# Kernel tuning notes

Hardware: AMD Instinct MI355X
Metric: run time of the kernel (lower is better)

The kernel has to match this reference:

```python
import jax, jax.numpy as jnp
import numpy as np
import math

D_MODEL = 1024
N_HEAD = 16
D_HEAD = D_MODEL // N_HEAD


def setup_inputs() -> dict:
    key = jax.random.key(0)
    k0, k1, k2, k3, k4 = jax.random.split(key, 5)
    B, N = 4, 2048
    inp = jax.random.normal(k0, (B, N, D_MODEL), dtype=jnp.float32)
    # causal mask: True = keep (masked_fill on ~mask)
    mask = jnp.tril(jnp.ones((N, N), dtype=bool))
    # qkv_proj Linear(d_model, 3*d_model); output Linear(d_model, d_model)
    s_in = 1.0 / math.sqrt(D_MODEL)
    W_qkv = jax.random.uniform(k1, (D_MODEL, 3 * D_MODEL), jnp.float32, -s_in, s_in)
    b_qkv = jax.random.uniform(k2, (3 * D_MODEL,), jnp.float32, -s_in, s_in)
    W_out = jax.random.uniform(k3, (D_MODEL, D_MODEL), jnp.float32, -s_in, s_in)
    b_out = jax.random.uniform(k4, (D_MODEL,), jnp.float32, -s_in, s_in)
    return {"input": inp, "W_qkv": W_qkv, "b_qkv": b_qkv,
            "W_out": W_out, "b_out": b_out, "mask": mask}


def reference(input, W_qkv, b_qkv, W_out, b_out, mask):
    B, N, d = input.shape
    qkv = input @ W_qkv + b_qkv                       # [B,N,3d]  (dropout=eval no-op)
    q, k, v = jnp.split(qkv, 3, axis=-1)
    # [B,N,H,Dh] -> [B,H,N,Dh]
    q = q.reshape(B, N, N_HEAD, D_HEAD).transpose(0, 2, 1, 3)
    k = k.reshape(B, N, N_HEAD, D_HEAD).transpose(0, 2, 1, 3)
    v = v.reshape(B, N, N_HEAD, D_HEAD).transpose(0, 2, 1, 3)
    scale = 1.0 / math.sqrt(D_HEAD)
    scores = jnp.einsum('bhqd,bhkd->bhqk', q, k) * scale   # [B,H,N,N]
    scores = jnp.where(mask, scores, -jnp.inf)
    attn = jax.nn.softmax(scores, axis=-1)
    out = jnp.einsum('bhqk,bhkd->bhqd', attn, v)           # [B,H,N,Dh]
    out = out.transpose(0, 2, 1, 3).reshape(B, N, d)       # concat heads
    return out @ W_out + b_out
```

## Files before the change

### kernel.cpp

```cpp
#include <hip/hip_runtime.h>
#include <hip/hip_bf16.h>

typedef unsigned short u16;
typedef unsigned u32;
typedef __attribute__((ext_vector_type(4))) unsigned short u16x4;
typedef __attribute__((ext_vector_type(8))) unsigned short u16x8;
typedef __attribute__((ext_vector_type(4))) unsigned u32x4;
typedef __attribute__((ext_vector_type(8))) __bf16 bf16x8;
typedef __attribute__((ext_vector_type(4))) float f32x4;

typedef __attribute__((address_space(1))) void as1v;
typedef __attribute__((address_space(3))) void as3v;

#define MFMA16(a, b, c) __builtin_amdgcn_mfma_f32_16x16x32_bf16(a, b, c, 0, 0, 0)

#if __has_builtin(__builtin_amdgcn_permlane16_swap) && __has_builtin(__builtin_amdgcn_permlane32_swap)
#define HAVE_PERMLANE_SWAP 1
#else
#define HAVE_PERMLANE_SWAP 0
#endif

__device__ __forceinline__ u16 f2bf(float f) {
    unsigned u = __builtin_bit_cast(unsigned, f);
    u += 0x7fffu + ((u >> 16) & 1u);
    return (u16)(u >> 16);
}

__device__ __forceinline__ float bf2f(u16 v) {
    u32 u = ((u32)v) << 16;
    return __builtin_bit_cast(float, u);
}

__device__ __forceinline__ u32 pkbf(float lo, float hi) {
    u32 r;
    asm("v_cvt_pk_bf16_f32 %0, %1, %2" : "=v"(r) : "v"(lo), "v"(hi));
    return r;
}

__device__ __forceinline__ void gload16(const void* g, void* l) {
    __builtin_amdgcn_global_load_lds((as1v*)g, (as3v*)l, 16, 0, 0);
}

__device__ __forceinline__ float redmax_cross(float v) {
#if HAVE_PERMLANE_SWAP
    u32 xu = __builtin_bit_cast(u32, v);
    auto r16 = __builtin_amdgcn_permlane16_swap(xu, xu, false, false);
    float a = fmaxf(__builtin_bit_cast(float, (u32)r16[0]),
                    __builtin_bit_cast(float, (u32)r16[1]));
    u32 au = __builtin_bit_cast(u32, a);
    auto r32 = __builtin_amdgcn_permlane32_swap(au, au, false, false);
    return fmaxf(__builtin_bit_cast(float, (u32)r32[0]),
                 __builtin_bit_cast(float, (u32)r32[1]));
#else
    v = fmaxf(v, __shfl_xor(v, 16, 64));
    return fmaxf(v, __shfl_xor(v, 32, 64));
#endif
}

__device__ __forceinline__ float redsum_cross(float v) {
#if HAVE_PERMLANE_SWAP
    u32 xu = __builtin_bit_cast(u32, v);
    auto r16 = __builtin_amdgcn_permlane16_swap(xu, xu, false, false);
    float a = __builtin_bit_cast(float, (u32)r16[0]) +
              __builtin_bit_cast(float, (u32)r16[1]);
    u32 au = __builtin_bit_cast(u32, a);
    auto r32 = __builtin_amdgcn_permlane32_swap(au, au, false, false);
    return __builtin_bit_cast(float, (u32)r32[0]) +
           __builtin_bit_cast(float, (u32)r32[1]);
#else
    v += __shfl_xor(v, 16, 64);
    return v + __shfl_xor(v, 32, 64);
#endif
}

__global__ void convert_f32_bf16(const float* __restrict__ in, u16* __restrict__ out, int n4) {
    int i = blockIdx.x * blockDim.x + threadIdx.x;
    if (i < n4) {
        float4 v = *(const float4*)&in[(size_t)i * 4];
        u16x4 o;
        o.x = f2bf(v.x); o.y = f2bf(v.y); o.z = f2bf(v.z); o.w = f2bf(v.w);
        *(u16x4*)&out[(size_t)i * 4] = o;
    }
}

__global__ void transpose_convert(const float* __restrict__ in, u16* __restrict__ out, int R, int C) {
    __shared__ float tl[64][65];
    const int rb = blockIdx.x, cb = blockIdx.y;
    const int tid = threadIdx.x;
    for (int it = 0; it < 4; ++it) {
        int lin = (tid + it * 256) * 4;
        int r = lin >> 6, c = lin & 63;
        float4 v = *(const float4*)&in[(size_t)(rb * 64 + r) * C + cb * 64 + c];
        tl[r][c + 0] = v.x; tl[r][c + 1] = v.y; tl[r][c + 2] = v.z; tl[r][c + 3] = v.w;
    }
    __syncthreads();
    for (int it = 0; it < 4; ++it) {
        int lin = (tid + it * 256) * 4;
        int oc = lin >> 6, orr = lin & 63;
        u16x4 o;
        o.x = f2bf(tl[orr + 0][oc]);
        o.y = f2bf(tl[orr + 1][oc]);
        o.z = f2bf(tl[orr + 2][oc]);
        o.w = f2bf(tl[orr + 3][oc]);
        *(u16x4*)&out[(size_t)(cb * 64 + oc) * R + rb * 64 + orr] = o;
    }
}

__global__ __launch_bounds__(256, 3) void gemm128_qkv(
    const u16* __restrict__ A, const u16* __restrict__ Bt, const float* __restrict__ bias,
    u16* __restrict__ qb, u16* __restrict__ kb, u16* __restrict__ vtb) {
    constexpr int K = 1024;
    constexpr int NT = 32;
    __shared__ u16 ldsu[24576];

    const int bid = blockIdx.x;
    const int s = (bid & 7) * 192 + (bid >> 3);
    const int bm = s / 24, bn = s % 24;

    const int tid = threadIdx.x, wid = tid >> 6, lane = tid & 63;
    const int wr = wid >> 1, wc = wid & 1;
    const int l15 = lane & 15, lhi = lane >> 4;

    const int sslot = (lane & 7) ^ (lane >> 3);
    const int kcol = (sslot & 3) * 8;
    const int mloc = (lane >> 3) * 2 + (sslot >> 2);

    const u16* Arow[2];
    const u16* Brow[2];
#pragma unroll
    for (int li = 0; li < 2; ++li) {
        int sg = wid * 2 + li;
        Arow[li] = A + (size_t)(bm * 128 + sg * 16 + mloc) * K + kcol;
        Brow[li] = Bt + (size_t)(bn * 128 + sg * 16 + mloc) * K + kcol;
    }

    auto stageA = [&](int buf, int t) {
#pragma unroll
        for (int li = 0; li < 2; ++li) {
            int sg = wid * 2 + li;
            gload16(Arow[li] + t * 32, (char*)ldsu + buf * 16384 + sg * 1024);
        }
    };
    auto stageB = [&](int buf, int t) {
#pragma unroll
        for (int li = 0; li < 2; ++li) {
            int sg = wid * 2 + li;
            gload16(Brow[li] + t * 32, (char*)ldsu + buf * 16384 + 8192 + sg * 1024);
        }
    };

    const int rslot = ((l15 & 1) * 4 + lhi) ^ ((l15 >> 1) & 7);
    const int fragoff = (l15 >> 1) * 64 + rslot * 8;

    f32x4 acc[4][4];
#pragma unroll
    for (int i = 0; i < 4; ++i)
#pragma unroll
        for (int j = 0; j < 4; ++j) acc[i][j] = (f32x4){0.f, 0.f, 0.f, 0.f};

    auto doTile = [&](int cur, int tstage, bool dostage) {
        const u16* Ab = ldsu + cur * 8192 + wr * 2048 + fragoff;
        const u16* Bb = ldsu + cur * 8192 + 4096 + wc * 2048 + fragoff;
        bf16x8 af[4], b0, b1;
#pragma unroll
        for (int mf = 0; mf < 4; ++mf) af[mf] = *(const bf16x8*)(Ab + mf * 512);
        b0 = *(const bf16x8*)(Bb);
        b1 = *(const bf16x8*)(Bb + 512);
        if (dostage) stageA(tstage % 3, tstage);
        __builtin_amdgcn_s_setprio(1);
#pragma unroll
        for (int mf = 0; mf < 4; ++mf) {
            acc[mf][0] = MFMA16(af[mf], b0, acc[mf][0]);
            acc[mf][1] = MFMA16(af[mf], b1, acc[mf][1]);
        }
        __builtin_amdgcn_s_setprio(0);
        b0 = *(const bf16x8*)(Bb + 1024);
        b1 = *(const bf16x8*)(Bb + 1536);
        if (dostage) stageB(tstage % 3, tstage);
        __builtin_amdgcn_s_setprio(1);
#pragma unroll
        for (int mf = 0; mf < 4; ++mf) {
            acc[mf][2] = MFMA16(af[mf], b0, acc[mf][2]);
            acc[mf][3] = MFMA16(af[mf], b1, acc[mf][3]);
        }
        __builtin_amdgcn_s_setprio(0);
    };

    stageA(0, 0); stageB(0, 0);
    stageA(1, 1); stageB(1, 1);
    asm volatile("s_waitcnt vmcnt(4)" ::: "memory");
    __builtin_amdgcn_s_barrier();
    __builtin_amdgcn_sched_barrier(0);

    for (int t = 0; t < NT - 2; ++t) {
        doTile(t % 3, t + 2, true);
        asm volatile("s_waitcnt vmcnt(4)" ::: "memory");
        __builtin_amdgcn_s_barrier();
        __builtin_amdgcn_sched_barrier(0);
    }
    doTile((NT - 2) % 3, 0, false);
    asm volatile("s_waitcnt vmcnt(0)" ::: "memory");
    __builtin_amdgcn_s_barrier();
    __builtin_amdgcn_sched_barrier(0);
    doTile((NT - 1) % 3, 0, false);

    const int cg0 = bn * 128 + wc * 64;
    const int which = cg0 >> 10, rem = cg0 & 1023;
    const int hh = rem >> 6, dh0 = rem & 63;
    const int rgb0 = bm * 128 + wr * 64;
    const int bb = rgb0 >> 11, n0 = rgb0 & 2047;

    if (which == 2) {
        const size_t vbase = ((size_t)(bb * 16 + hh) * 64 + dh0) * 2048 + (size_t)n0;
#pragma unroll
        for (int nt = 0; nt < 4; ++nt) {
            float bv = bias[cg0 + nt * 16 + l15];
            size_t rowb = vbase + (size_t)(nt * 16 + l15) * 2048;
#pragma unroll
            for (int mt = 0; mt < 4; ++mt) {
                u16x4 w;
#pragma unroll
                for (int v = 0; v < 4; ++v) w[v] = f2bf(acc[mt][nt][v] + bv);
                *(u16x4*)&vtb[rowb + mt * 16 + lhi * 4] = w;
            }
        }
    } else {
        u16* dst = (which == 0) ? qb : kb;
        const float qs = (which == 0) ? 0.18033688011112042f : 1.0f;
        const size_t gbase = (((size_t)bb * 16 + hh) * 2048 + n0) * 64 + dh0;
#pragma unroll
        for (int nt = 0; nt < 4; ++nt) {
            float bv = bias[cg0 + nt * 16 + l15];
#pragma unroll
            for (int mt = 0; mt < 4; ++mt)
#pragma unroll
                for (int v = 0; v < 4; ++v) {
                    int n = mt * 16 + lhi * 4 + v;
                    dst[gbase + (size_t)n * 64 + nt * 16 + l15] =
                        f2bf((acc[mt][nt][v] + bv) * qs);
                }
        }
    }
}

__global__ __launch_bounds__(512, 2) void gemm256_out(
    const u16* __restrict__ A, const u16* __restrict__ Bt, const float* __restrict__ bias,
    float* __restrict__ outf) {
    constexpr int K = 1024;
    constexpr int NT = 32;
    __shared__ u16 ldsu[49152];

    const int bid = blockIdx.x;
    const int swz = (bid & 7) * 32 + (bid >> 3);
    const int bm = swz >> 3, bn = swz & 7;

    const int tid = threadIdx.x, wid = tid >> 6, lane = tid & 63;
    const int wr = wid >> 2, wc = wid & 3;
    const int l15 = lane & 15, lhi = lane >> 4;

    const int sslot = (lane & 7) ^ (lane >> 3);
    const int kcol = (sslot & 3) * 8;
    const int mloc = (lane >> 3) * 2 + (sslot >> 2);

    const u16* Arow[2];
#pragma unroll
    for (int li = 0; li < 2; ++li) {
        int sg = wid * 2 + li;
        Arow[li] = A + (size_t)(bm * 256 + sg * 16 + mloc) * K + kcol;
    }
    const u16* Brow = Bt + (size_t)(bn * 128 + wid * 16 + mloc) * K + kcol;

    auto stageA = [&](int buf, int t) {
#pragma unroll
        for (int li = 0; li < 2; ++li) {
            int sg = wid * 2 + li;
            gload16(Arow[li] + t * 32, (char*)ldsu + buf * 24576 + sg * 1024);
        }
    };
    auto stageB = [&](int buf, int t) {
        gload16(Brow + t * 32, (char*)ldsu + buf * 24576 + 16384 + wid * 1024);
    };

    const int rslot = ((l15 & 1) * 4 + lhi) ^ ((l15 >> 1) & 7);
    const int fragoff = (l15 >> 1) * 64 + rslot * 8;

    f32x4 acc[8][2];
#pragma unroll
    for (int i = 0; i < 8; ++i) {
        acc[i][0] = (f32x4){0.f, 0.f, 0.f, 0.f};
        acc[i][1] = (f32x4){0.f, 0.f, 0.f, 0.f};
    }

    auto doTile = [&](int cur, int tstage, bool dostage) {
        const u16* Ab = ldsu + cur * 12288 + wr * 4096 + fragoff;
        const u16* Bb = ldsu + cur * 12288 + 8192 + wc * 1024 + fragoff;
        bf16x8 af[8], b0, b1;
#pragma unroll
        for (int mf = 0; mf < 8; ++mf) af[mf] = *(const bf16x8*)(Ab + mf * 512);
        b0 = *(const bf16x8*)(Bb);
        b1 = *(const bf16x8*)(Bb + 512);
        if (dostage) stageA(tstage & 3, tstage);
        __builtin_amdgcn_s_setprio(1);
#pragma unroll
        for (int mf = 0; mf < 8; ++mf) acc[mf][0] = MFMA16(af[mf], b0, acc[mf][0]);
        __builtin_amdgcn_s_setprio(0);
        if (dostage) stageB(tstage & 3, tstage);
        __builtin_amdgcn_s_setprio(1);
#pragma unroll
        for (int mf = 0; mf < 8; ++mf) acc[mf][1] = MFMA16(af[mf], b1, acc[mf][1]);
        __builtin_amdgcn_s_setprio(0);
    };

    stageA(0, 0); stageB(0, 0);
    stageA(1, 1); stageB(1, 1);
    stageA(2, 2); stageB(2, 2);
    asm volatile("s_waitcnt vmcnt(6)" ::: "memory");
    __builtin_amdgcn_s_barrier();
    __builtin_amdgcn_sched_barrier(0);

    for (int t = 0; t < NT - 3; ++t) {
        doTile(t & 3, t + 3, true);
        asm volatile("s_waitcnt vmcnt(6)" ::: "memory");
        __builtin_amdgcn_s_barrier();
        __builtin_amdgcn_sched_barrier(0);
    }
    doTile((NT - 3) & 3, 0, false);
    asm volatile("s_waitcnt vmcnt(3)" ::: "memory");
    __builtin_amdgcn_s_barrier();
    __builtin_amdgcn_sched_barrier(0);
    doTile((NT - 2) & 3, 0, false);
    asm volatile("s_waitcnt vmcnt(0)" ::: "memory");
    __builtin_amdgcn_s_barrier();
    __builtin_amdgcn_sched_barrier(0);
    doTile((NT - 1) & 3, 0, false);

#pragma unroll
    for (int nf = 0; nf < 2; ++nf) {
        int cg = bn * 128 + wc * 32 + nf * 16 + l15;
        float bv = bias[cg];
#pragma unroll
        for (int mf = 0; mf < 8; ++mf) {
            int rgb = bm * 256 + wr * 128 + mf * 16 + lhi * 4;
#pragma unroll
            for (int v = 0; v < 4; ++v)
                outf[(size_t)(rgb + v) * 1024 + cg] = acc[mf][nf][v] + bv;
        }
    }
}

__global__ __launch_bounds__(256, 4) void attn_kernel(
    const u16* __restrict__ qbuf, const u16* __restrict__ kbuf,
    const u16* __restrict__ vtb, u16* __restrict__ obuf,
    float* __restrict__ pbufA, float* __restrict__ mlbuf) {
    __shared__ u16 Kl[2][64 * 64];
    __shared__ u16 Vl[2][64 * 64];
    const int bid = blockIdx.x;
    const int bh = ((bid & 7) << 3) + ((bid >> 3) & 7);
    const int piece = bid >> 6;
    const int half = piece & 1;
    const int p = piece >> 1;
    const int b = bh >> 4, h = bh & 15;
    const int tid = threadIdx.x, wid = tid >> 6, lane = tid & 63;
    const int l15 = lane & 15, lhi = lane >> 4;

    const int srow = lane >> 3;
    const int scolb = ((lane & 7) * 16) ^ (srow << 4);

    auto stage = [&](int buf, int t) {
        const int kbase = t * 64;
#pragma unroll
        for (int s = 0; s < 2; ++s) {
            int sg = wid * 2 + s;
            int row = sg * 8 + srow;
            const u16* gk = kbuf + ((size_t)bh * 2048 + kbase + row) * 64 + (scolb >> 1);
            gload16(gk, (char*)Kl[buf] + sg * 1024);
            const u16* gv = vtb + ((size_t)bh * 64 + row) * 2048 + kbase + (scolb >> 1);
            gload16(gv, (char*)Vl[buf] + sg * 1024);
        }
    };

    auto run_piece = [&](int c, int t0, int t1, int mode) {
        const int q0 = c * 128 + wid * 32;
        bf16x8 qf0[2], qf1[2];
        {
            const u16* qp0 = qbuf + ((size_t)bh * 2048 + q0 + l15) * 64 + lhi * 8;
            const u16* qp1 = qbuf + ((size_t)bh * 2048 + q0 + 16 + l15) * 64 + lhi * 8;
            qf0[0] = *(const bf16x8*)(qp0); qf0[1] = *(const bf16x8*)(qp0 + 32);
            qf1[0] = *(const bf16x8*)(qp1); qf1[1] = *(const bf16x8*)(qp1 + 32);
        }
        float m0 = -1e30f, l0 = 0.f, m1 = -1e30f, l1 = 0.f;
        f32x4 o0[4], o1[4];
#pragma unroll
        for (int d = 0; d < 4; ++d) {
            o0[d] = (f32x4){0.f, 0.f, 0.f, 0.f};
            o1[d] = (f32x4){0.f, 0.f, 0.f, 0.f};
        }
        const int ntW = 2 * c + (wid >> 1) + 1;

        auto smax = [&](f32x4* s, int qg0, int t, float& m, float& l, f32x4* oa, u32* pw) {
            const int qg = qg0 + l15;
            if (64 * t + 63 > qg0) {
#pragma unroll
                for (int kb4 = 0; kb4 < 4; ++kb4)
#pragma unroll
                    for (int v = 0; v < 4; ++v) {
                        int kg = 64 * t + kb4 * 16 + lhi * 4 + v;
                        if (kg > qg) s[kb4][v] = -1e30f;
                    }
            }
            float pm = fmaxf(fmaxf(fmaxf(s[0][0], s[0][1]), fmaxf(s[0][2], s[0][3])),
                             fmaxf(fmaxf(s[1][0], s[1][1]), fmaxf(s[1][2], s[1][3])));
            pm = fmaxf(pm, fmaxf(fmaxf(fmaxf(s[2][0], s[2][1]), fmaxf(s[2][2], s[2][3])),
                                 fmaxf(fmaxf(s[3][0], s[3][1]), fmaxf(s[3][2], s[3][3]))));
            pm = redmax_cross(pm);
            if (!__all(pm <= m + 8.f)) {
                float nm = fmaxf(m, pm);
                float f = exp2f(m - nm);
                m = nm;
                l *= f;
#pragma unroll
                for (int d = 0; d < 4; ++d)
#pragma unroll
                    for (int v = 0; v < 4; ++v) oa[d][v] *= f;
            }
            float rs = 0.f;
#pragma unroll
            for (int kb4 = 0; kb4 < 4; ++kb4)
#pragma unroll
                for (int v = 0; v < 4; ++v) {
                    float e = exp2f(s[kb4][v] - m);
                    s[kb4][v] = e;
                    rs += e;
                }
            l += redsum_cross(rs);
            pw[0] = pkbf(s[0][0], s[0][1]); pw[1] = pkbf(s[0][2], s[0][3]);
            pw[2] = pkbf(s[1][0], s[1][1]); pw[3] = pkbf(s[1][2], s[1][3]);
            pw[4] = pkbf(s[2][0], s[2][1]); pw[5] = pkbf(s[2][2], s[2][3]);
            pw[6] = pkbf(s[3][0], s[3][1]); pw[7] = pkbf(s[3][2], s[3][3]);
        };

        auto computeChunk = [&](const char* Kb, const char* Vb, int t) {
            f32x4 s0[4], s1[4];
            __builtin_amdgcn_s_setprio(1);
#pragma unroll
            for (int kb4 = 0; kb4 < 4; ++kb4) {
                const int r = kb4 * 16 + l15;
                const int sw = (r & 7) << 4;
                const int rowb = r * 128;
                bf16x8 kf0 = *(const bf16x8*)(Kb + rowb + ((lhi * 16) ^ sw));
                bf16x8 kf1 = *(const bf16x8*)(Kb + rowb + ((64 + lhi * 16) ^ sw));
                f32x4 a0 = (f32x4){0.f, 0.f, 0.f, 0.f};
                a0 = MFMA16(kf0, qf0[0], a0);
                a0 = MFMA16(kf1, qf0[1], a0);
                s0[kb4] = a0;
                f32x4 a1 = (f32x4){0.f, 0.f, 0.f, 0.f};
                a1 = MFMA16(kf0, qf1[0], a1);
                a1 = MFMA16(kf1, qf1[1], a1);
                s1[kb4] = a1;
            }
            __builtin_amdgcn_s_setprio(0);
            u32 pw0[8], pw1[8];
            smax(s0, q0, t, m0, l0, o0, pw0);
            smax(s1, q0 + 16, t, m1, l1, o1, pw1);
            __builtin_amdgcn_s_setprio(1);
#pragma unroll
            for (int ks = 0; ks < 2; ++ks) {
                bf16x8 pb0 = __builtin_bit_cast(bf16x8,
                    (u32x4){pw0[ks * 4 + 0], pw0[ks * 4 + 1], pw0[ks * 4 + 2], pw0[ks * 4 + 3]});
                bf16x8 pb1 = __builtin_bit_cast(bf16x8,
                    (u32x4){pw1[ks * 4 + 0], pw1[ks * 4 + 1], pw1[ks * 4 + 2], pw1[ks * 4 + 3]});
#pragma unroll
                for (int dhb = 0; dhb < 4; ++dhb) {
                    const int r = dhb * 16 + l15;
                    const int sw = (r & 7) << 4;
                    u16x4 v0 = *(const u16x4*)(Vb + r * 128 + ((ks * 64 + 8 * lhi) ^ sw));
                    u16x4 v1 = *(const u16x4*)(Vb + r * 128 + ((ks * 64 + 32 + 8 * lhi) ^ sw));
                    u16x8 vv = {v0[0], v0[1], v0[2], v0[3], v1[0], v1[1], v1[2], v1[3]};
                    bf16x8 vf = __builtin_bit_cast(bf16x8, vv);
                    o0[dhb] = MFMA16(vf, pb0, o0[dhb]);
                    o1[dhb] = MFMA16(vf, pb1, o1[dhb]);
                }
            }
            __builtin_amdgcn_s_setprio(0);
        };

        __syncthreads();
        stage(0, t0);
        int t = t0;
        for (;;) {
            __syncthreads();
            if (t + 1 < t1) stage(((t - t0) & 1) ^ 1, t + 1);
            if (t < ntW) computeChunk((const char*)Kl[(t - t0) & 1],
                                      (const char*)Vl[(t - t0) & 1], t);
            if (++t == t1) break;
        }

        const int pi = 15 - c;
        if (mode == 0) {
            auto epi = [&](int goff, float l, const f32x4* oa) {
                const float rl = 1.f / l;
                const int q = q0 + goff + l15;
                const size_t rowoff = ((size_t)b * 2048 + q) * 1024 + h * 64;
#pragma unroll
                for (int dhb = 0; dhb < 4; ++dhb) {
                    u16x4 w;
#pragma unroll
                    for (int v = 0; v < 4; ++v) w[v] = f2bf(oa[dhb][v] * rl);
                    *(u16x4*)&obuf[rowoff + dhb * 16 + lhi * 4] = w;
                }
            };
            epi(0, l0, o0);
            epi(16, l1, o1);
        } else if (mode == 1) {
            auto epi = [&](int goff, float m, float l, const f32x4* oa) {
                const int ql = wid * 32 + goff + l15;
                const size_t rowi = ((size_t)bh * 8 + pi) * 128 + ql;
                float* prow = pbufA + rowi * 64;
#pragma unroll
                for (int dhb = 0; dhb < 4; ++dhb)
                    *(f32x4*)&prow[dhb * 16 + lhi * 4] = oa[dhb];
                if (lhi == 0) { mlbuf[rowi] = m; mlbuf[65536 + rowi] = l; }
            };
            epi(0, m0, l0, o0);
            epi(16, m1, l1, o1);
        } else {
            auto epi = [&](int goff, float m, float l, const f32x4* oa) {
                const float rl = 1.f / l;
                const int q = q0 + goff + l15;
                const size_t rowoff = ((size_t)b * 2048 + q) * 1024 + h * 64;
#pragma unroll
                for (int dhb = 0; dhb < 4; ++dhb) {
                    u16x4 w;
#pragma unroll
                    for (int v = 0; v < 4; ++v) w[v] = f2bf(oa[dhb][v] * rl);
                    *(u16x4*)&obuf[rowoff + dhb * 16 + lhi * 4] = w;
                }
                const int ql = wid * 32 + goff + l15;
                const size_t rowi = ((size_t)bh * 8 + pi) * 128 + ql;
                if (lhi == 0) { mlbuf[131072 + rowi] = m; mlbuf[196608 + rowi] = l; }
            };
            epi(0, m0, l0, o0);
            epi(16, m1, l1, o1);
        }
    };

    if (half == 0) {
        run_piece(p, 0, 2 * p + 2, 0);
        run_piece(15 - p, 0, 15 - 2 * p, 1);
    } else {
        run_piece(15 - p, 15 - 2 * p, 32 - 2 * p, 2);
    }
}

__global__ __launch_bounds__(256) void merge_lse(
    const float* __restrict__ pbufA, const float* __restrict__ mlbuf,
    u16* __restrict__ obuf) {
    const int gid = blockIdx.x * 256 + threadIdx.x;
    const int rid = gid >> 2, seg = gid & 3;
    const float m1 = mlbuf[rid], l1 = mlbuf[65536 + rid];
    const float m2 = mlbuf[131072 + rid], l2 = mlbuf[196608 + rid];
    const float M = fmaxf(m1, m2);
    const float f1 = exp2f(m1 - M), f2 = exp2f(m2 - M);
    const float rden = 1.f / (l1 * f1 + l2 * f2);
    const float w2 = l2 * f2;
    const int bh = rid >> 10, rem = rid & 1023, pp = rem >> 7, ql = rem & 127;
    const int b = bh >> 4, h = bh & 15;
    const int qg = (15 - pp) * 128 + ql;
    u16* orow = obuf + ((size_t)b * 2048 + qg) * 1024 + h * 64 + seg * 16;
    const float* prow = pbufA + (size_t)rid * 64 + seg * 16;
#pragma unroll
    for (int j = 0; j < 4; ++j) {
        f32x4 o1 = *(const f32x4*)&prow[j * 4];
        u16x4 o2 = *(const u16x4*)&orow[j * 4];
        u16x4 w;
#pragma unroll
        for (int v = 0; v < 4; ++v)
            w[v] = f2bf((o1[v] * f1 + bf2f(o2[v]) * w2) * rden);
        *(u16x4*)&orow[j * 4] = w;
    }
}

extern "C" void kernel_launch(void* const* d_in, const int* in_sizes, int n_in,
                              void* d_out, int out_size, void* d_ws, size_t ws_size,
                              hipStream_t stream) {
    const float* inp   = (const float*)d_in[0];
    const float* W_qkv = (const float*)d_in[1];
    const float* b_qkv = (const float*)d_in[2];
    const float* W_out = (const float*)d_in[3];
    const float* b_out = (const float*)d_in[4];
    float* out = (float*)d_out;

    u16* xb   = (u16*)d_ws;
    u16* wqt  = xb + 8388608;
    u16* wot  = wqt + 3145728;
    u16* qbuf = wot + 1048576;
    u16* kbuf = qbuf + 8388608;
    u16* vtb  = kbuf + 8388608;
    u16* obuf = vtb + 8388608;
    float* pbufA = (float*)xb;
    float* mlbuf = (float*)wqt;

    convert_f32_bf16<<<8192, 256, 0, stream>>>(inp, xb, 2097152);
    transpose_convert<<<dim3(16, 48), 256, 0, stream>>>(W_qkv, wqt, 1024, 3072);
    transpose_convert<<<dim3(16, 16), 256, 0, stream>>>(W_out, wot, 1024, 1024);
    gemm128_qkv<<<1536, 256, 0, stream>>>(xb, wqt, b_qkv, qbuf, kbuf, vtb);
    attn_kernel<<<1024, 256, 0, stream>>>(qbuf, kbuf, vtb, obuf, pbufA, mlbuf);
    merge_lse<<<1024, 256, 0, stream>>>(pbufA, mlbuf, obuf);
    gemm256_out<<<256, 512, 0, stream>>>(obuf, wot, b_out, out);
}
```

Measured before the change: 201.6 us.

## Retile output GEMM to 128x128 blocks and store attention partials in bf16

The output projection GEMM moves from 256x128 tiles with 512 threads and 4 LDS buffers to 128x128 tiles with 256 threads, 3 LDS buffers and twice as many blocks. The aim is better occupancy and load balance across CUs. The split-attention partial outputs are now written as bf16 instead of fp32, which halves that traffic between the attention and merge kernels. Non-temporal loads and stores are used on these scratch buffers, at some precision cost for the partial accumulator.

After: 201.2 us. About the same (-0.2%).

```diff
diff --git a/kernel.cpp b/kernel.cpp
--- a/kernel.cpp
+++ b/kernel.cpp
@@ -243,19 +243,19 @@
     }
 }
 
-__global__ __launch_bounds__(512, 2) void gemm256_out(
+__global__ __launch_bounds__(256, 3) void gemm128_out(
     const u16* __restrict__ A, const u16* __restrict__ Bt, const float* __restrict__ bias,
     float* __restrict__ outf) {
     constexpr int K = 1024;
     constexpr int NT = 32;
-    __shared__ u16 ldsu[49152];
+    __shared__ u16 ldsu[24576];
 
     const int bid = blockIdx.x;
-    const int swz = (bid & 7) * 32 + (bid >> 3);
-    const int bm = swz >> 3, bn = swz & 7;
+    const int s = (bid & 7) * 64 + (bid >> 3);
+    const int bm = s >> 3, bn = s & 7;
 
     const int tid = threadIdx.x, wid = tid >> 6, lane = tid & 63;
-    const int wr = wid >> 2, wc = wid & 3;
+    const int wr = wid >> 1, wc = wid & 1;
     const int l15 = lane & 15, lhi = lane >> 4;
 
     const int sslot = (lane & 7) ^ (lane >> 3);
@@ -263,87 +263,94 @@
     const int mloc = (lane >> 3) * 2 + (sslot >> 2);
 
     const u16* Arow[2];
+    const u16* Brow[2];
 #pragma unroll
     for (int li = 0; li < 2; ++li) {
         int sg = wid * 2 + li;
-        Arow[li] = A + (size_t)(bm * 256 + sg * 16 + mloc) * K + kcol;
-    }
-    const u16* Brow = Bt + (size_t)(bn * 128 + wid * 16 + mloc) * K + kcol;
+        Arow[li] = A + (size_t)(bm * 128 + sg * 16 + mloc) * K + kcol;
+        Brow[li] = Bt + (size_t)(bn * 128 + sg * 16 + mloc) * K + kcol;
+    }
 
     auto stageA = [&](int buf, int t) {
 #pragma unroll
         for (int li = 0; li < 2; ++li) {
             int sg = wid * 2 + li;
-            gload16(Arow[li] + t * 32, (char*)ldsu + buf * 24576 + sg * 1024);
+            gload16(Arow[li] + t * 32, (char*)ldsu + buf * 16384 + sg * 1024);
         }
     };
     auto stageB = [&](int buf, int t) {
-        gload16(Brow + t * 32, (char*)ldsu + buf * 24576 + 16384 + wid * 1024);
+#pragma unroll
+        for (int li = 0; li < 2; ++li) {
+            int sg = wid * 2 + li;
+            gload16(Brow[li] + t * 32, (char*)ldsu + buf * 16384 + 8192 + sg * 1024);
+        }
     };
 
     const int rslot = ((l15 & 1) * 4 + lhi) ^ ((l15 >> 1) & 7);
     const int fragoff = (l15 >> 1) * 64 + rslot * 8;
 
-    f32x4 acc[8][2];
-#pragma unroll
-    for (int i = 0; i < 8; ++i) {
-        acc[i][0] = (f32x4){0.f, 0.f, 0.f, 0.f};
-        acc[i][1] = (f32x4){0.f, 0.f, 0.f, 0.f};
-    }
+    f32x4 acc[4][4];
+#pragma unroll
+    for (int i = 0; i < 4; ++i)
+#pragma unroll
+        for (int j = 0; j < 4; ++j) acc[i][j] = (f32x4){0.f, 0.f, 0.f, 0.f};
 
     auto doTile = [&](int cur, int tstage, bool dostage) {
-        const u16* Ab = ldsu + cur * 12288 + wr * 4096 + fragoff;
-        const u16* Bb = ldsu + cur * 12288 + 8192 + wc * 1024 + fragoff;
-        bf16x8 af[8], b0, b1;
-#pragma unroll
-        for (int mf = 0; mf < 8; ++mf) af[mf] = *(const bf16x8*)(Ab + mf * 512);
+        const u16* Ab = ldsu + cur * 8192 + wr * 2048 + fragoff;
+        const u16* Bb = ldsu + cur * 8192 + 4096 + wc * 2048 + fragoff;
+        bf16x8 af[4], b0, b1;
+#pragma unroll
+        for (int mf = 0; mf < 4; ++mf) af[mf] = *(const bf16x8*)(Ab + mf * 512);
         b0 = *(const bf16x8*)(Bb);
         b1 = *(const bf16x8*)(Bb + 512);
-        if (dostage) stageA(tstage & 3, tstage);
+        if (dostage) stageA(tstage % 3, tstage);
         __builtin_amdgcn_s_setprio(1);
 #pragma unroll
-        for (int mf = 0; mf < 8; ++mf) acc[mf][0] = MFMA16(af[mf], b0, acc[mf][0]);
+        for (int mf = 0; mf < 4; ++mf) {
+            acc[mf][0] = MFMA16(af[mf], b0, acc[mf][0]);
+            acc[mf][1] = MFMA16(af[mf], b1, acc[mf][1]);
+        }
         __builtin_amdgcn_s_setprio(0);
-        if (dostage) stageB(tstage & 3, tstage);
+        b0 = *(const bf16x8*)(Bb + 1024);
+        b1 = *(const bf16x8*)(Bb + 1536);
+        if (dostage) stageB(tstage % 3, tstage);
         __builtin_amdgcn_s_setprio(1);
 #pragma unroll
-        for (int mf = 0; mf < 8; ++mf) acc[mf][1] = MFMA16(af[mf], b1, acc[mf][1]);
+        for (int mf = 0; mf < 4; ++mf) {
+            acc[mf][2] = MFMA16(af[mf], b0, acc[mf][2]);
+            acc[mf][3] = MFMA16(af[mf], b1, acc[mf][3]);
+        }
         __builtin_amdgcn_s_setprio(0);
     };
 
     stageA(0, 0); stageB(0, 0);
     stageA(1, 1); stageB(1, 1);
-    stageA(2, 2); stageB(2, 2);
-    asm volatile("s_waitcnt vmcnt(6)" ::: "memory");
+    asm volatile("s_waitcnt vmcnt(4)" ::: "memory");
     __builtin_amdgcn_s_barrier();
     __builtin_amdgcn_sched_barrier(0);
 
-    for (int t = 0; t < NT - 3; ++t) {
-        doTile(t & 3, t + 3, true);
-        asm volatile("s_waitcnt vmcnt(6)" ::: "memory");
+    for (int t = 0; t < NT - 2; ++t) {
+        doTile(t % 3, t + 2, true);
+        asm volatile("s_waitcnt vmcnt(4)" ::: "memory");
         __builtin_amdgcn_s_barrier();
         __builtin_amdgcn_sched_barrier(0);
     }
-    doTile((NT - 3) & 3, 0, false);
-    asm volatile("s_waitcnt vmcnt(3)" ::: "memory");
-    __builtin_amdgcn_s_barrier();
-    __builtin_amdgcn_sched_barrier(0);
-    doTile((NT - 2) & 3, 0, false);
+    doTile((NT - 2) % 3, 0, false);
     asm volatile("s_waitcnt vmcnt(0)" ::: "memory");
     __builtin_amdgcn_s_barrier();
     __builtin_amdgcn_sched_barrier(0);
-    doTile((NT - 1) & 3, 0, false);
-
-#pragma unroll
-    for (int nf = 0; nf < 2; ++nf) {
-        int cg = bn * 128 + wc * 32 + nf * 16 + l15;
+    doTile((NT - 1) % 3, 0, false);
+
+#pragma unroll
+    for (int nt = 0; nt < 4; ++nt) {
+        int cg = bn * 128 + wc * 64 + nt * 16 + l15;
         float bv = bias[cg];
 #pragma unroll
-        for (int mf = 0; mf < 8; ++mf) {
-            int rgb = bm * 256 + wr * 128 + mf * 16 + lhi * 4;
+        for (int mt = 0; mt < 4; ++mt) {
+            int rg = bm * 128 + wr * 64 + mt * 16 + lhi * 4;
 #pragma unroll
             for (int v = 0; v < 4; ++v)
-                outf[(size_t)(rgb + v) * 1024 + cg] = acc[mf][nf][v] + bv;
+                outf[(size_t)(rg + v) * 1024 + cg] = acc[mt][nt][v] + bv;
         }
     }
 }
@@ -351,7 +358,7 @@
 __global__ __launch_bounds__(256, 4) void attn_kernel(
     const u16* __restrict__ qbuf, const u16* __restrict__ kbuf,
     const u16* __restrict__ vtb, u16* __restrict__ obuf,
-    float* __restrict__ pbufA, float* __restrict__ mlbuf) {
+    u16* __restrict__ pbufA, float* __restrict__ mlbuf) {
     __shared__ u16 Kl[2][64 * 64];
     __shared__ u16 Vl[2][64 * 64];
     const int bid = blockIdx.x;
@@ -515,11 +522,18 @@
             auto epi = [&](int goff, float m, float l, const f32x4* oa) {
                 const int ql = wid * 32 + goff + l15;
                 const size_t rowi = ((size_t)bh * 8 + pi) * 128 + ql;
-                float* prow = pbufA + rowi * 64;
-#pragma unroll
-                for (int dhb = 0; dhb < 4; ++dhb)
-                    *(f32x4*)&prow[dhb * 16 + lhi * 4] = oa[dhb];
-                if (lhi == 0) { mlbuf[rowi] = m; mlbuf[65536 + rowi] = l; }
+                u16* prow = pbufA + rowi * 64;
+#pragma unroll
+                for (int dhb = 0; dhb < 4; ++dhb) {
+                    u16x4 w;
+#pragma unroll
+                    for (int v = 0; v < 4; ++v) w[v] = f2bf(oa[dhb][v]);
+                    __builtin_nontemporal_store(w, (u16x4*)&prow[dhb * 16 + lhi * 4]);
+                }
+                if (lhi == 0) {
+                    __builtin_nontemporal_store(m, &mlbuf[rowi]);
+                    __builtin_nontemporal_store(l, &mlbuf[65536 + rowi]);
+                }
             };
             epi(0, m0, l0, o0);
             epi(16, m1, l1, o1);
@@ -537,7 +551,10 @@
                 }
                 const int ql = wid * 32 + goff + l15;
                 const size_t rowi = ((size_t)bh * 8 + pi) * 128 + ql;
-                if (lhi == 0) { mlbuf[131072 + rowi] = m; mlbuf[196608 + rowi] = l; }
+                if (lhi == 0) {
+                    __builtin_nontemporal_store(m, &mlbuf[131072 + rowi]);
+                    __builtin_nontemporal_store(l, &mlbuf[196608 + rowi]);
+                }
             };
             epi(0, m0, l0, o0);
             epi(16, m1, l1, o1);
@@ -553,12 +570,14 @@
 }
 
 __global__ __launch_bounds__(256) void merge_lse(
-    const float* __restrict__ pbufA, const float* __restrict__ mlbuf,
+    const u16* __restrict__ pbufA, const float* __restrict__ mlbuf,
     u16* __restrict__ obuf) {
     const int gid = blockIdx.x * 256 + threadIdx.x;
     const int rid = gid >> 2, seg = gid & 3;
-    const float m1 = mlbuf[rid], l1 = mlbuf[65536 + rid];
-    const float m2 = mlbuf[131072 + rid], l2 = mlbuf[196608 + rid];
+    const float m1 = __builtin_nontemporal_load(&mlbuf[rid]);
+    const float l1 = __builtin_nontemporal_load(&mlbuf[65536 + rid]);
+    const float m2 = __builtin_nontemporal_load(&mlbuf[131072 + rid]);
+    const float l2 = __builtin_nontemporal_load(&mlbuf[196608 + rid]);
     const float M = fmaxf(m1, m2);
     const float f1 = exp2f(m1 - M), f2 = exp2f(m2 - M);
     const float rden = 1.f / (l1 * f1 + l2 * f2);
@@ -567,15 +586,15 @@
     const int b = bh >> 4, h = bh & 15;
     const int qg = (15 - pp) * 128 + ql;
     u16* orow = obuf + ((size_t)b * 2048 + qg) * 1024 + h * 64 + seg * 16;
-    const float* prow = pbufA + (size_t)rid * 64 + seg * 16;
+    const u16* prow = pbufA + (size_t)rid * 64 + seg * 16;
 #pragma unroll
     for (int j = 0; j < 4; ++j) {
-        f32x4 o1 = *(const f32x4*)&prow[j * 4];
+        u16x4 p1 = __builtin_nontemporal_load((const u16x4*)&prow[j * 4]);
         u16x4 o2 = *(const u16x4*)&orow[j * 4];
         u16x4 w;
 #pragma unroll
         for (int v = 0; v < 4; ++v)
-            w[v] = f2bf((o1[v] * f1 + bf2f(o2[v]) * w2) * rden);
+            w[v] = f2bf((bf2f(p1[v]) * f1 + bf2f(o2[v]) * w2) * rden);
         *(u16x4*)&orow[j * 4] = w;
     }
 }
@@ -597,7 +616,7 @@
     u16* kbuf = qbuf + 8388608;
     u16* vtb  = kbuf + 8388608;
     u16* obuf = vtb + 8388608;
-    float* pbufA = (float*)xb;
+    u16* pbufA = xb;
     float* mlbuf = (float*)wqt;
 
     convert_f32_bf16<<<8192, 256, 0, stream>>>(inp, xb, 2097152);
@@ -606,5 +625,5 @@
     gemm128_qkv<<<1536, 256, 0, stream>>>(xb, wqt, b_qkv, qbuf, kbuf, vtb);
     attn_kernel<<<1024, 256, 0, stream>>>(qbuf, kbuf, vtb, obuf, pbufA, mlbuf);
     merge_lse<<<1024, 256, 0, stream>>>(pbufA, mlbuf, obuf);
-    gemm256_out<<<256, 512, 0, stream>>>(obuf, wot, b_out, out);
-}
+    gemm128_out<<<512, 256, 0, stream>>>(obuf, wot, b_out, out);
+}
```
